# Optimization experiments

Hardware: AMD Instinct MI355X
Metric: run time of the kernel (lower is better)

## Reference

```python
import jax, jax.numpy as jnp
import numpy as np
from jax import lax

B, T, E, H, V = 1024, 128, 300, 100, 50000
K = 4  # topk in catch()
NEG_INF = -1e30


def setup_inputs() -> dict:
    key = jax.random.key(0)
    ks = jax.random.split(key, 12)
    word_id = jax.random.randint(ks[0], (B, T), 0, V, dtype=jnp.int32)
    sen_len = jax.random.randint(ks[1], (B,), K, T + 1, dtype=jnp.int32)  # >= K for topk
    label_word_id = jax.random.randint(ks[2], (B, 1), 0, V, dtype=jnp.int32)
    emb = jax.random.normal(ks[3], (V, E), jnp.float32) * 0.1
    W_ih = jax.random.normal(ks[4], (4 * H, E), jnp.float32) * 0.05
    W_hh = jax.random.normal(ks[5], (4 * H, H), jnp.float32) * 0.05
    b_ih = jax.random.normal(ks[6], (4 * H,), jnp.float32) * 0.05
    b_hh = jax.random.normal(ks[7], (4 * H,), jnp.float32) * 0.05
    lin_W = jax.random.normal(ks[8], (6, H), jnp.float32) * 0.1
    lin_b = jax.random.normal(ks[9], (6,), jnp.float32) * 0.1
    ll_W = jax.random.normal(ks[10], (H, E), jnp.float32) * 0.05
    ll_b = jax.random.normal(ks[11], (H,), jnp.float32) * 0.05
    return dict(word_id=word_id, sen_len=sen_len, label_word_id=label_word_id,
                emb=emb, W_ih=W_ih, W_hh=W_hh, b_ih=b_ih, b_hh=b_hh,
                lin_W=lin_W, lin_b=lin_b, ll_W=ll_W, ll_b=ll_b)


def _lstm(x, W_ih, W_hh, b_ih, b_hh):
    # x: (B, T, E) -> out: (B, T, H). Single layer, pytorch gate order i,f,g,o.
    b = b_ih + b_hh
    def step(carry, x_t):
        h, c = carry
        gates = x_t @ W_ih.T + h @ W_hh.T + b  # (B, 4H)
        i, f, g, o = jnp.split(gates, 4, axis=-1)
        c = jax.nn.sigmoid(f) * c + jax.nn.sigmoid(i) * jnp.tanh(g)
        h = jax.nn.sigmoid(o) * jnp.tanh(c)
        return (h, c), h
    h0 = jnp.zeros((x.shape[0], W_hh.shape[1]), x.dtype)
    (_, _), hs = lax.scan(step, (h0, h0), x.transpose(1, 0, 2))
    return hs.transpose(1, 0, 2)


def reference(word_id, sen_len, label_word_id, emb, W_ih, W_hh, b_ih, b_hh,
              lin_W, lin_b, ll_W, ll_b):
    word_vec = emb[word_id]                      # (B, T, E)
    out = _lstm(word_vec, W_ih, W_hh, b_ih, b_hh)  # (B, T, H)

    # last valid hidden state -> linear
    last = out[jnp.arange(out.shape[0]), sen_len - 1]  # (B, H)
    out_f = last @ lin_W.T + lin_b               # (B, 6)

    # label vector through llinear
    label_vec = emb[label_word_id[:, 0]] @ ll_W.T + ll_b  # (B, H)

    # --- catch(), vectorized ---
    scores = jnp.einsum('bth,bh->bt', out, label_vec)     # (B, T)
    valid = jnp.arange(out.shape[1])[None, :] < sen_len[:, None]  # (B, T)
    vals, idx = lax.top_k(jnp.where(valid, scores, NEG_INF), K)   # (B, K)
    s_value = jnp.take_along_axis(out, idx[:, :, None], axis=1)   # (B, K, H)
    pos = jnp.sum(s_value * vals[:, :, None], axis=1)             # (B, H)

    # neg: valid positions excluding topk; original bug: vector_list accumulates
    # across the batch loop -> cumulative sum over batch dimension.
    top_mask = jnp.zeros(valid.shape, bool).at[
        jnp.arange(valid.shape[0])[:, None], idx].set(True)
    neg_mask = valid & ~top_mask                                   # (B, T)
    per_neg = jnp.einsum('bth,bt->bh', out, neg_mask.astype(out.dtype))
    neg = jnp.cumsum(per_neg, axis=0)                              # (B, H)

    l_rep = pos @ lin_W.T + lin_b
    r_rep = neg @ lin_W.T + lin_b
    return (out_f, l_rep, r_rep)
```

## Files before the change

kernel.cpp:

```cpp
#include <hip/hip_runtime.h>
#include <hip/hip_bf16.h>
#include <cstdint>

#define Bn   1024
#define Tn   128
#define En   300
#define Hn   100
#define Vn   50000
#define G4n  400
#define MPn  50048
#define NPn  448

typedef __bf16 bf16x8 __attribute__((ext_vector_type(8)));
typedef _Float16 half8 __attribute__((ext_vector_type(8)));
typedef _Float16 half2v __attribute__((ext_vector_type(2)));
typedef float  f32x4  __attribute__((ext_vector_type(4)));

#define OFF_TABLE  0ull
#define OFF_OH16   44800000ull
#define OFF_WFRAG  71014400ull
#define OFF_WFRAGB 71129088ull
#define OFF_LLWT   71415808ull
#define OFF_LV     71535808ull
#define OFF_PN     71945408ull
#define OFF_NEG    72355008ull

__device__ __forceinline__ float sigf(float x) { return 1.0f / (1.0f + __expf(-x)); }
__device__ __forceinline__ float tanhfast(float x) { return 1.0f - 2.0f / (__expf(2.0f * x) + 1.0f); }

#define BAR_LDS() do {                                         \
    asm volatile("s_waitcnt lgkmcnt(0)" ::: "memory");          \
    __builtin_amdgcn_s_barrier();                               \
    asm volatile("" ::: "memory");                              \
} while (0)

#define DPP_ADD_SHL(v, N) do {                                                     \
    int _s = __builtin_amdgcn_update_dpp(0, __builtin_bit_cast(int, (v)),          \
                                         0x100 | (N), 0xF, 0xF, true);             \
    (v) += __builtin_bit_cast(float, _s);                                          \
} while (0)

__global__ void k_prep(const float* __restrict__ W_ih, const float* __restrict__ W_hh,
                       const float* __restrict__ llW,
                       uint4* __restrict__ wfrag, uint4* __restrict__ wfragB,
                       float* __restrict__ llwt) {
    int idx = blockIdx.x * 256 + threadIdx.x;
    if (idx < 28 * 4 * 64) {
        int lane = idx & 63, tk = idx >> 6;
        int nt = tk >> 2, kc = tk & 3;
        int n = nt * 16 + (lane & 15);
        int k0 = kc * 32 + (lane >> 4) * 8;
        int q = n & 3, u = n >> 2;
        union { _Float16 h[8]; uint4 v; } pk;
#pragma unroll
        for (int j = 0; j < 8; j++) {
            int k = k0 + j;
            pk.h[j] = (_Float16)((u < Hn && k < Hn) ? W_hh[(size_t)(q * Hn + u) * Hn + k] : 0.0f);
        }
        wfrag[idx] = pk.v;
    }
    if (idx < 10 * 28 * 64) {
        int lane = idx & 63, tk = idx >> 6;
        int kc = tk / 28, nsg = tk - kc * 28;
        int n = nsg * 16 + (lane & 15);
        int k0 = kc * 32 + (lane >> 4) * 8;
        int q = n & 3, u = n >> 2;
        union { __bf16 h[8]; uint4 v; } pk;
#pragma unroll
        for (int j = 0; j < 8; j++) {
            int k = k0 + j;
            pk.h[j] = (__bf16)((u < Hn && k < En) ? W_ih[(size_t)(q * Hn + u) * En + k] : 0.0f);
        }
        wfragB[idx] = pk.v;
    }
    if (idx < En * Hn) {
        int k = idx / Hn, h = idx - k * Hn;
        llwt[idx] = llW[(size_t)h * En + k];
    }
}

__global__ __launch_bounds__(256, 2) void k_table(
    const float* __restrict__ emb, const uint4* __restrict__ wfragB,
    const float* __restrict__ b_ih, const float* __restrict__ b_hh,
    _Float16* __restrict__ table) {
    __shared__ __bf16 a_sh[64][328];
    const int tid = threadIdx.x;
    const int mt = blockIdx.x >> 1, nh = blockIdx.x & 1;

#pragma unroll
    for (int it = 0; it < 5; it++) {
        int x = it * 256 + tid;
        int row = x / 20, seg = x - row * 20;
        int gr = mt * 64 + row;
        const float* ar = emb + (size_t)(gr < Vn ? gr : Vn - 1) * En;
        int c0 = seg * 16;
        union { __bf16 h[16]; bf16x8 v[2]; } pk;
#pragma unroll
        for (int g = 0; g < 4; g++) {
            int c = c0 + g * 4;
            if (c + 4 <= En) {
                float4 f = *(const float4*)(ar + c);
                pk.h[g * 4 + 0] = (__bf16)f.x; pk.h[g * 4 + 1] = (__bf16)f.y;
                pk.h[g * 4 + 2] = (__bf16)f.z; pk.h[g * 4 + 3] = (__bf16)f.w;
            } else {
                pk.h[g * 4 + 0] = (__bf16)0.f; pk.h[g * 4 + 1] = (__bf16)0.f;
                pk.h[g * 4 + 2] = (__bf16)0.f; pk.h[g * 4 + 3] = (__bf16)0.f;
            }
        }
        *(bf16x8*)&a_sh[row][c0] = pk.v[0];
        *(bf16x8*)&a_sh[row][c0 + 8] = pk.v[1];
    }
    __syncthreads();

    const int wv = tid >> 6, l = tid & 63;
    const int c16 = l & 15, quad = l >> 4;
    f32x4 acc[14];
#pragma unroll
    for (int i = 0; i < 14; i++) acc[i] = (f32x4){0.f, 0.f, 0.f, 0.f};

    uint4 bcur[14];
#pragma unroll
    for (int ns = 0; ns < 14; ns++) bcur[ns] = wfragB[((0 * 28 + nh * 14 + ns) << 6) + l];

    for (int kc = 0; kc < 10; kc++) {
        uint4 bnxt[14];
        if (kc < 9) {
#pragma unroll
            for (int ns = 0; ns < 14; ns++) bnxt[ns] = wfragB[(((kc + 1) * 28 + nh * 14 + ns) << 6) + l];
        }
        bf16x8 af = *(const bf16x8*)&a_sh[wv * 16 + c16][kc * 32 + quad * 8];
#pragma unroll
        for (int ns = 0; ns < 14; ns++)
            acc[ns] = __builtin_amdgcn_mfma_f32_16x16x32_bf16(af, __builtin_bit_cast(bf16x8, bcur[ns]), acc[ns], 0, 0, 0);
        if (kc < 9) {
#pragma unroll
            for (int ns = 0; ns < 14; ns++) bcur[ns] = bnxt[ns];
        }
    }
#pragma unroll
    for (int ns = 0; ns < 14; ns++) {
        int n = (nh * 14 + ns) * 16 + c16;
        int q = n & 3, u = n >> 2;
        if (u < Hn) {
            int j = q * Hn + u;
            float bias = b_ih[j] + b_hh[j];
#pragma unroll
            for (int r = 0; r < 4; r++) {
                int m = mt * 64 + wv * 16 + quad * 4 + r;
                if (m < Vn) table[(size_t)m * NPn + n] = (_Float16)(acc[ns][r] + bias);
            }
        }
    }
}

__global__ void k_label(const int* __restrict__ lwid, const float* __restrict__ emb,
                        const float* __restrict__ llwt, const float* __restrict__ llb,
                        float* __restrict__ lv) {
    __shared__ float er[En];
    __shared__ float part[Hn];
    int b = blockIdx.x;
    int lid = lwid[b];
    for (int k = threadIdx.x; k < En; k += 256) er[k] = emb[(size_t)lid * En + k];
    __syncthreads();
    int h = threadIdx.x & 127, half = threadIdx.x >> 7;
    float acc = 0.f;
    if (h < Hn) {
        int k0 = half * 150, k1 = k0 + 150;
        for (int k = k0; k < k1; k++) acc += er[k] * llwt[k * Hn + h];
        if (half == 1) part[h] = acc;
    }
    __syncthreads();
    if (h < Hn && half == 0) lv[(size_t)b * Hn + h] = acc + part[h] + llb[h];
}

__global__ __launch_bounds__(256, 2) void k_lstm(
    const int* __restrict__ word_id, const int* __restrict__ sen_len,
    const _Float16* __restrict__ table, const uint4* __restrict__ wfrag,
    const float* __restrict__ lv, const float* __restrict__ linW,
    const float* __restrict__ linb, _Float16* __restrict__ oh16,
    float* __restrict__ per_neg, float* __restrict__ d_out) {
    __shared__ float    gbufs[4][280];
    __shared__ _Float16 h_cur[2][2][136];
    __shared__ float    spw[2][Tn][16];
    __shared__ int      widc[2][Tn];
    __shared__ float    pos_sh[2][Hn];
    __shared__ float    lasth_sh[2][Hn];
    __shared__ float    tk_val[2][4];
    __shared__ int      tk_idx[2][4];

    const int tid = threadIdx.x;
    const int w = tid >> 6, l = tid & 63;
    const int c16 = l & 15, quad = l >> 4;
    const int b0 = blockIdx.x * 2;

    for (int i = tid; i < 272; i += 256) ((uint32_t*)h_cur)[i] = 0u;
    { int imb = tid >> 7, it = tid & 127; widc[imb][it] = word_id[(b0 + imb) * Tn + it]; }

    half8 bfr[7][4];
#pragma unroll
    for (int n7 = 0; n7 < 7; n7++)
#pragma unroll
        for (int kc = 0; kc < 4; kc++)
            bfr[n7][kc] = __builtin_bit_cast(half8, wfrag[((w * 7 + n7) * 4 + kc) * 64 + l]);

    const int u_loc = l >> 1, mb = l & 1;
    const int u = w * 28 + u_loc;
    const bool act = (l < 56) && (u < Hn);
    const int myslen = act ? sen_len[b0 + mb] : 0;
    const float lt_reg = act ? lv[(size_t)(b0 + mb) * Hn + u] : 0.f;
    float* gb = &gbufs[w][0];

    __syncthreads();

    uint2 xq = {0, 0}, xq1 = {0, 0};
    if (act) {
        xq  = *(const uint2*)(table + (size_t)widc[mb][0] * NPn + u * 4);
        xq1 = *(const uint2*)(table + (size_t)widc[mb][1] * NPn + u * 4);
    }

    float c_reg = 0.f, sumh = 0.f, lasth = 0.f;
    float p_carry = 0.f;
    _Float16* ohb_w = oh16 + (size_t)(b0 + mb) * Tn * Hn;

    for (int t = 0; t < Tn; t++) {
        const _Float16* hp = &h_cur[t & 1][0][0];
        f32x4 acc[7];
#pragma unroll
        for (int n7 = 0; n7 < 7; n7++) acc[n7] = (f32x4){0.f, 0.f, 0.f, 0.f};
#pragma unroll
        for (int kc = 0; kc < 4; kc++) {
            half8 af = *(const half8*)(hp + (c16 & 1) * 136 + kc * 32 + quad * 8);
#pragma unroll
            for (int n7 = 0; n7 < 7; n7++)
                acc[n7] = __builtin_amdgcn_mfma_f32_16x16x32_f16(af, bfr[n7][kc], acc[n7], 0, 0, 0);
        }
        {
            float pr = p_carry;
            DPP_ADD_SHL(pr, 2);
            DPP_ADD_SHL(pr, 4);
            DPP_ADD_SHL(pr, 8);
            if ((l & 15) < 2 && t > 0) spw[l & 1][t - 1][w * 4 + quad] = pr;
        }
        if (l < 16) {
#pragma unroll
            for (int n7 = 0; n7 < 7; n7++) {
                int nl = n7 * 16 + l;
                int adr = (nl >> 2) * 5 + (nl & 3);
                gb[adr] = acc[n7][0];
                gb[140 + adr] = acc[n7][1];
            }
        }
        float p = 0.f;
        if (act) {
            int base = mb * 140 + u_loc * 5;
            half2v x01 = __builtin_bit_cast(half2v, xq.x);
            half2v x23 = __builtin_bit_cast(half2v, xq.y);
            float gi = gb[base] + (float)x01.x;
            float gf = gb[base + 1] + (float)x01.y;
            float gg = gb[base + 2] + (float)x23.x;
            float go = gb[base + 3] + (float)x23.y;
            float c = sigf(gf) * c_reg + sigf(gi) * tanhfast(gg);
            c_reg = c;
            float hh = sigf(go) * tanhfast(c);
            h_cur[(t + 1) & 1][mb][u] = (_Float16)hh;
            ohb_w[t * Hn + u] = (_Float16)hh;
            if (t < myslen) sumh += hh;
            if (t == myslen - 1) lasth = hh;
            p = hh * lt_reg;
            int tn2 = (t + 2 < Tn) ? t + 2 : Tn - 1;
            xq = xq1;
            xq1 = *(const uint2*)(table + (size_t)widc[mb][tn2] * NPn + u * 4);
        }
        p_carry = p;
        BAR_LDS();
    }
    {
        float pr = p_carry;
        DPP_ADD_SHL(pr, 2);
        DPP_ADD_SHL(pr, 4);
        DPP_ADD_SHL(pr, 8);
        if ((l & 15) < 2) spw[l & 1][Tn - 1][w * 4 + quad] = pr;
    }
    __syncthreads();
    if (w < 2) {
        int kmb = w, lane = l;
        int sl = sen_len[b0 + kmb];
        const float* s16a = &spw[kmb][lane][0];
        const float* s16b = &spw[kmb][lane + 64][0];
        float4 a0 = *(const float4*)(s16a + 0), a1 = *(const float4*)(s16a + 4);
        float4 a2 = *(const float4*)(s16a + 8), a3 = *(const float4*)(s16a + 12);
        float4 b0v = *(const float4*)(s16b + 0), b1v = *(const float4*)(s16b + 4);
        float4 b2v = *(const float4*)(s16b + 8), b3v = *(const float4*)(s16b + 12);
        float sa = (a0.x + a0.y + a0.z + a0.w) + (a1.x + a1.y + a1.z + a1.w)
                 + (a2.x + a2.y + a2.z + a2.w) + (a3.x + a3.y + a3.z + a3.w);
        float sb = (b0v.x + b0v.y + b0v.z + b0v.w) + (b1v.x + b1v.y + b1v.z + b1v.w)
                 + (b2v.x + b2v.y + b2v.z + b2v.w) + (b3v.x + b3v.y + b3v.z + b3v.w);
        float s0 = (lane < sl) ? sa : -1e30f;
        float s1 = (lane + 64 < sl) ? sb : -1e30f;
        bool tk0 = false, tk1 = false;
#pragma unroll
        for (int p4 = 0; p4 < 4; p4++) {
            float v = tk0 ? -1e30f : s0;
            int ix = lane;
            float v1 = tk1 ? -1e30f : s1;
            if (v1 > v) { v = v1; ix = lane + 64; }
            for (int off = 32; off; off >>= 1) {
                float ov = __shfl_down(v, off, 64);
                int oi = __shfl_down(ix, off, 64);
                if (ov > v || (ov == v && oi < ix)) { v = ov; ix = oi; }
            }
            v = __shfl(v, 0, 64);
            ix = __shfl(ix, 0, 64);
            if (lane == 0) { tk_val[kmb][p4] = v; tk_idx[kmb][p4] = ix; }
            if (ix == lane) tk0 = true;
            if (ix == lane + 64) tk1 = true;
        }
    }
    __syncthreads();
    if (act) {
        float pos = 0.f, nsum = sumh;
#pragma unroll
        for (int p4 = 0; p4 < 4; p4++) {
            int ix = tk_idx[mb][p4];
            float r = (float)ohb_w[ix * Hn + u];
            pos += tk_val[mb][p4] * r;
            nsum -= r;
        }
        pos_sh[mb][u] = pos;
        lasth_sh[mb][u] = lasth;
        per_neg[(size_t)(b0 + mb) * Hn + u] = nsum;
    }
    __syncthreads();
    if (tid < 24) {
        int which = tid / 12, r = tid - which * 12;
        int pmb = r / 6, o = r - pmb * 6;
        const float* src = which ? &pos_sh[pmb][0] : &lasth_sh[pmb][0];
        float acc2 = linb[o];
        for (int uu = 0; uu < Hn; uu++) acc2 += src[uu] * linW[o * Hn + uu];
        d_out[(which ? (Bn * 6) : 0) + (b0 + pmb) * 6 + o] = acc2;
    }
}

__global__ __launch_bounds__(1024) void k_scan(const float* __restrict__ pn, float* __restrict__ neg) {
    __shared__ float wsum[16];
    __shared__ float wpre[16];
    int u = blockIdx.x, t = threadIdx.x;
    int lane = t & 63, wv = t >> 6;
    float v = pn[(size_t)t * Hn + u];
#pragma unroll
    for (int off = 1; off < 64; off <<= 1) {
        float o = __shfl_up(v, off, 64);
        if (lane >= off) v += o;
    }
    if (lane == 63) wsum[wv] = v;
    __syncthreads();
    if (t < 16) {
        float s = wsum[t];
#pragma unroll
        for (int off = 1; off < 16; off <<= 1) {
            float o = __shfl_up(s, off, 64);
            if (t >= off) s += o;
        }
        wpre[t] = s;
    }
    __syncthreads();
    float pre = wv ? wpre[wv - 1] : 0.f;
    neg[(size_t)t * Hn + u] = v + pre;
}

__global__ void k_rrep(const float* __restrict__ neg, const float* __restrict__ linW,
                       const float* __restrict__ linb, float* __restrict__ d_out) {
    int gid = blockIdx.x * 256 + threadIdx.x;
    if (gid < Bn * 6) {
        int b = gid / 6, o = gid - b * 6;
        float acc = linb[o];
        for (int u = 0; u < Hn; u++) acc += neg[(size_t)b * Hn + u] * linW[o * Hn + u];
        d_out[2 * Bn * 6 + gid] = acc;
    }
}

extern "C" void kernel_launch(void* const* d_in, const int* in_sizes, int n_in,
                              void* d_out, int out_size, void* d_ws, size_t ws_size,
                              hipStream_t stream) {
    const int*   word_id = (const int*)d_in[0];
    const int*   sen_len = (const int*)d_in[1];
    const int*   lwid    = (const int*)d_in[2];
    const float* emb     = (const float*)d_in[3];
    const float* W_ih    = (const float*)d_in[4];
    const float* W_hh    = (const float*)d_in[5];
    const float* b_ih    = (const float*)d_in[6];
    const float* b_hh    = (const float*)d_in[7];
    const float* linW    = (const float*)d_in[8];
    const float* linb    = (const float*)d_in[9];
    const float* llW     = (const float*)d_in[10];
    const float* llb     = (const float*)d_in[11];

    char* ws = (char*)d_ws;
    _Float16* table  = (_Float16*)(ws + OFF_TABLE);
    _Float16* oh16   = (_Float16*)(ws + OFF_OH16);
    uint4*    wfrag  = (uint4*)(ws + OFF_WFRAG);
    uint4*    wfragB = (uint4*)(ws + OFF_WFRAGB);
    float*    llwt   = (float*)(ws + OFF_LLWT);
    float*    lvp    = (float*)(ws + OFF_LV);
    float*    pn     = (float*)(ws + OFF_PN);
    float*    neg    = (float*)(ws + OFF_NEG);
    float*    outp   = (float*)d_out;

    k_prep<<<118, 256, 0, stream>>>(W_ih, W_hh, llW, wfrag, wfragB, llwt);
    k_table<<<(MPn / 64) * 2, 256, 0, stream>>>(emb, wfragB, b_ih, b_hh, table);
    k_label<<<Bn, 256, 0, stream>>>(lwid, emb, llwt, llb, lvp);
    k_lstm<<<Bn / 2, 256, 0, stream>>>(word_id, sen_len, table, wfrag, lvp, linW, linb, oh16, pn, outp);
    k_scan<<<Hn, 1024, 0, stream>>>(pn, neg);
    k_rrep<<<(Bn * 6 + 255) / 256, 256, 0, stream>>>(neg, linW, linb, outp);
}
```

Before: 309.1 us.

## Process four sequences per LSTM block to fill more MFMA rows

Each k_lstm block now handles four batch rows instead of two. It uses more rows of the 16-row MFMA A operand and halves the block count to 256, which fits one block per CU on a 256-CU part. Each active lane now runs the gate math for two sequences per timestep. The score buffer is transposed for the top-k reduction, and all four waves now do top-k. A large dummy shared array, written only under an impossible condition, forces LDS use up so blocks get one per CU. The cost is double the serial gate work per lane on the recurrent critical path.

```diff
diff --git a/kernel.cpp b/kernel.cpp
--- a/kernel.cpp
+++ b/kernel.cpp
@@ -173,28 +173,32 @@
     if (h < Hn && half == 0) lv[(size_t)b * Hn + h] = acc + part[h] + llb[h];
 }
 
-__global__ __launch_bounds__(256, 2) void k_lstm(
+__global__ __launch_bounds__(256, 1) void k_lstm(
     const int* __restrict__ word_id, const int* __restrict__ sen_len,
     const _Float16* __restrict__ table, const uint4* __restrict__ wfrag,
     const float* __restrict__ lv, const float* __restrict__ linW,
     const float* __restrict__ linb, _Float16* __restrict__ oh16,
     float* __restrict__ per_neg, float* __restrict__ d_out) {
-    __shared__ float    gbufs[4][280];
-    __shared__ _Float16 h_cur[2][2][136];
-    __shared__ float    spw[2][Tn][16];
-    __shared__ int      widc[2][Tn];
-    __shared__ float    pos_sh[2][Hn];
-    __shared__ float    lasth_sh[2][Hn];
-    __shared__ float    tk_val[2][4];
-    __shared__ int      tk_idx[2][4];
+    __shared__ float    gbufs[4][560];
+    __shared__ _Float16 h_cur[2][4][144];
+    __shared__ float    spw[4][16][132];
+    __shared__ int      widc[4][Tn];
+    __shared__ float    pos_sh[4][Hn];
+    __shared__ float    lasth_sh[4][Hn];
+    __shared__ float    tk_val[4][4];
+    __shared__ int      tk_idx[4][4];
+    __shared__ float    pad_force[9216];
 
     const int tid = threadIdx.x;
     const int w = tid >> 6, l = tid & 63;
     const int c16 = l & 15, quad = l >> 4;
-    const int b0 = blockIdx.x * 2;
-
-    for (int i = tid; i < 272; i += 256) ((uint32_t*)h_cur)[i] = 0u;
-    { int imb = tid >> 7, it = tid & 127; widc[imb][it] = word_id[(b0 + imb) * Tn + it]; }
+    const int b0 = blockIdx.x * 4;
+
+    if (__builtin_expect(sen_len[0] == -2147483647, 0)) pad_force[tid] = 1.f;
+
+    for (int i = tid; i < 576; i += 256) ((uint32_t*)h_cur)[i] = 0u;
+    for (int i = tid; i < 512; i += 256)
+        widc[i >> 7][i & 127] = word_id[(b0 + (i >> 7)) * Tn + (i & 127)];
 
     half8 bfr[7][4];
 #pragma unroll
@@ -203,24 +207,29 @@
         for (int kc = 0; kc < 4; kc++)
             bfr[n7][kc] = __builtin_bit_cast(half8, wfrag[((w * 7 + n7) * 4 + kc) * 64 + l]);
 
-    const int u_loc = l >> 1, mb = l & 1;
+    const int u_loc = l >> 1, sub = l & 1;
     const int u = w * 28 + u_loc;
     const bool act = (l < 56) && (u < Hn);
-    const int myslen = act ? sen_len[b0 + mb] : 0;
-    const float lt_reg = act ? lv[(size_t)(b0 + mb) * Hn + u] : 0.f;
+    const int slen_a = act ? sen_len[b0 + sub] : 0;
+    const int slen_b = act ? sen_len[b0 + sub + 2] : 0;
+    const float lt_a = act ? lv[(size_t)(b0 + sub) * Hn + u] : 0.f;
+    const float lt_b = act ? lv[(size_t)(b0 + sub + 2) * Hn + u] : 0.f;
     float* gb = &gbufs[w][0];
 
     __syncthreads();
 
-    uint2 xq = {0, 0}, xq1 = {0, 0};
+    uint2 xa0 = {0, 0}, xa1 = {0, 0}, xb0 = {0, 0}, xb1 = {0, 0};
     if (act) {
-        xq  = *(const uint2*)(table + (size_t)widc[mb][0] * NPn + u * 4);
-        xq1 = *(const uint2*)(table + (size_t)widc[mb][1] * NPn + u * 4);
-    }
-
-    float c_reg = 0.f, sumh = 0.f, lasth = 0.f;
-    float p_carry = 0.f;
-    _Float16* ohb_w = oh16 + (size_t)(b0 + mb) * Tn * Hn;
+        xa0 = *(const uint2*)(table + (size_t)widc[sub][0] * NPn + u * 4);
+        xa1 = *(const uint2*)(table + (size_t)widc[sub][1] * NPn + u * 4);
+        xb0 = *(const uint2*)(table + (size_t)widc[sub + 2][0] * NPn + u * 4);
+        xb1 = *(const uint2*)(table + (size_t)widc[sub + 2][1] * NPn + u * 4);
+    }
+
+    float ca = 0.f, cb = 0.f, sum_a = 0.f, sum_b = 0.f, last_a = 0.f, last_b = 0.f;
+    float pca = 0.f, pcb = 0.f;
+    _Float16* oha = oh16 + (size_t)(b0 + sub) * Tn * Hn;
+    _Float16* ohb = oh16 + (size_t)(b0 + sub + 2) * Tn * Hn;
 
     for (int t = 0; t < Tn; t++) {
         const _Float16* hp = &h_cur[t & 1][0][0];
@@ -229,81 +238,97 @@
         for (int n7 = 0; n7 < 7; n7++) acc[n7] = (f32x4){0.f, 0.f, 0.f, 0.f};
 #pragma unroll
         for (int kc = 0; kc < 4; kc++) {
-            half8 af = *(const half8*)(hp + (c16 & 1) * 136 + kc * 32 + quad * 8);
+            half8 af = *(const half8*)(hp + (c16 & 3) * 144 + kc * 32 + quad * 8);
 #pragma unroll
             for (int n7 = 0; n7 < 7; n7++)
                 acc[n7] = __builtin_amdgcn_mfma_f32_16x16x32_f16(af, bfr[n7][kc], acc[n7], 0, 0, 0);
         }
         {
-            float pr = p_carry;
-            DPP_ADD_SHL(pr, 2);
-            DPP_ADD_SHL(pr, 4);
-            DPP_ADD_SHL(pr, 8);
-            if ((l & 15) < 2 && t > 0) spw[l & 1][t - 1][w * 4 + quad] = pr;
+            float pra = pca, prb = pcb;
+            DPP_ADD_SHL(pra, 2); DPP_ADD_SHL(pra, 4); DPP_ADD_SHL(pra, 8);
+            DPP_ADD_SHL(prb, 2); DPP_ADD_SHL(prb, 4); DPP_ADD_SHL(prb, 8);
+            if ((l & 15) < 2 && t > 0) {
+                spw[l & 1][w * 4 + quad][t - 1] = pra;
+                spw[2 + (l & 1)][w * 4 + quad][t - 1] = prb;
+            }
         }
         if (l < 16) {
 #pragma unroll
             for (int n7 = 0; n7 < 7; n7++) {
                 int nl = n7 * 16 + l;
                 int adr = (nl >> 2) * 5 + (nl & 3);
-                gb[adr] = acc[n7][0];
+                gb[adr]       = acc[n7][0];
                 gb[140 + adr] = acc[n7][1];
+                gb[280 + adr] = acc[n7][2];
+                gb[420 + adr] = acc[n7][3];
             }
         }
-        float p = 0.f;
         if (act) {
-            int base = mb * 140 + u_loc * 5;
-            half2v x01 = __builtin_bit_cast(half2v, xq.x);
-            half2v x23 = __builtin_bit_cast(half2v, xq.y);
-            float gi = gb[base] + (float)x01.x;
-            float gf = gb[base + 1] + (float)x01.y;
-            float gg = gb[base + 2] + (float)x23.x;
-            float go = gb[base + 3] + (float)x23.y;
-            float c = sigf(gf) * c_reg + sigf(gi) * tanhfast(gg);
-            c_reg = c;
-            float hh = sigf(go) * tanhfast(c);
-            h_cur[(t + 1) & 1][mb][u] = (_Float16)hh;
-            ohb_w[t * Hn + u] = (_Float16)hh;
-            if (t < myslen) sumh += hh;
-            if (t == myslen - 1) lasth = hh;
-            p = hh * lt_reg;
+            int base = sub * 140 + u_loc * 5;
+            half2v a01 = __builtin_bit_cast(half2v, xa0.x);
+            half2v a23 = __builtin_bit_cast(half2v, xa0.y);
+            float gia = gb[base] + (float)a01.x;
+            float gfa = gb[base + 1] + (float)a01.y;
+            float gga = gb[base + 2] + (float)a23.x;
+            float goa = gb[base + 3] + (float)a23.y;
+            ca = sigf(gfa) * ca + sigf(gia) * tanhfast(gga);
+            float ha = sigf(goa) * tanhfast(ca);
+            h_cur[(t + 1) & 1][sub][u] = (_Float16)ha;
+            oha[t * Hn + u] = (_Float16)ha;
+            if (t < slen_a) sum_a += ha;
+            if (t == slen_a - 1) last_a = ha;
+            int baseb = base + 280;
+            half2v b01 = __builtin_bit_cast(half2v, xb0.x);
+            half2v b23 = __builtin_bit_cast(half2v, xb0.y);
+            float gib = gb[baseb] + (float)b01.x;
+            float gfb = gb[baseb + 1] + (float)b01.y;
+            float ggb = gb[baseb + 2] + (float)b23.x;
+            float gob = gb[baseb + 3] + (float)b23.y;
+            cb = sigf(gfb) * cb + sigf(gib) * tanhfast(ggb);
+            float hb = sigf(gob) * tanhfast(cb);
+            h_cur[(t + 1) & 1][sub + 2][u] = (_Float16)hb;
+            ohb[t * Hn + u] = (_Float16)hb;
+            if (t < slen_b) sum_b += hb;
+            if (t == slen_b - 1) last_b = hb;
+            pca = ha * lt_a;
+            pcb = hb * lt_b;
             int tn2 = (t + 2 < Tn) ? t + 2 : Tn - 1;
-            xq = xq1;
-            xq1 = *(const uint2*)(table + (size_t)widc[mb][tn2] * NPn + u * 4);
-        }
-        p_carry = p;
+            xa0 = xa1;
+            xa1 = *(const uint2*)(table + (size_t)widc[sub][tn2] * NPn + u * 4);
+            xb0 = xb1;
+            xb1 = *(const uint2*)(table + (size_t)widc[sub + 2][tn2] * NPn + u * 4);
+        } else {
+            pca = 0.f; pcb = 0.f;
+        }
         BAR_LDS();
     }
     {
-        float pr = p_carry;
-        DPP_ADD_SHL(pr, 2);
-        DPP_ADD_SHL(pr, 4);
-        DPP_ADD_SHL(pr, 8);
-        if ((l & 15) < 2) spw[l & 1][Tn - 1][w * 4 + quad] = pr;
-    }
-    __syncthreads();
-    if (w < 2) {
-        int kmb = w, lane = l;
-        int sl = sen_len[b0 + kmb];
-        const float* s16a = &spw[kmb][lane][0];
-        const float* s16b = &spw[kmb][lane + 64][0];
-        float4 a0 = *(const float4*)(s16a + 0), a1 = *(const float4*)(s16a + 4);
-        float4 a2 = *(const float4*)(s16a + 8), a3 = *(const float4*)(s16a + 12);
-        float4 b0v = *(const float4*)(s16b + 0), b1v = *(const float4*)(s16b + 4);
-        float4 b2v = *(const float4*)(s16b + 8), b3v = *(const float4*)(s16b + 12);
-        float sa = (a0.x + a0.y + a0.z + a0.w) + (a1.x + a1.y + a1.z + a1.w)
-                 + (a2.x + a2.y + a2.z + a2.w) + (a3.x + a3.y + a3.z + a3.w);
-        float sb = (b0v.x + b0v.y + b0v.z + b0v.w) + (b1v.x + b1v.y + b1v.z + b1v.w)
-                 + (b2v.x + b2v.y + b2v.z + b2v.w) + (b3v.x + b3v.y + b3v.z + b3v.w);
-        float s0 = (lane < sl) ? sa : -1e30f;
-        float s1 = (lane + 64 < sl) ? sb : -1e30f;
+        float pra = pca, prb = pcb;
+        DPP_ADD_SHL(pra, 2); DPP_ADD_SHL(pra, 4); DPP_ADD_SHL(pra, 8);
+        DPP_ADD_SHL(prb, 2); DPP_ADD_SHL(prb, 4); DPP_ADD_SHL(prb, 8);
+        if ((l & 15) < 2) {
+            spw[l & 1][w * 4 + quad][Tn - 1] = pra;
+            spw[2 + (l & 1)][w * 4 + quad][Tn - 1] = prb;
+        }
+    }
+    __syncthreads();
+    {
+        int sl = sen_len[b0 + w];
+        float s0 = 0.f, s1 = 0.f;
+#pragma unroll
+        for (int j = 0; j < 16; j++) {
+            s0 += spw[w][j][l];
+            s1 += spw[w][j][l + 64];
+        }
+        if (l >= sl) s0 = -1e30f;
+        if (l + 64 >= sl) s1 = -1e30f;
         bool tk0 = false, tk1 = false;
 #pragma unroll
         for (int p4 = 0; p4 < 4; p4++) {
             float v = tk0 ? -1e30f : s0;
-            int ix = lane;
+            int ix = l;
             float v1 = tk1 ? -1e30f : s1;
-            if (v1 > v) { v = v1; ix = lane + 64; }
+            if (v1 > v) { v = v1; ix = l + 64; }
             for (int off = 32; off; off >>= 1) {
                 float ov = __shfl_down(v, off, 64);
                 int oi = __shfl_down(ix, off, 64);
@@ -311,28 +336,36 @@
             }
             v = __shfl(v, 0, 64);
             ix = __shfl(ix, 0, 64);
-            if (lane == 0) { tk_val[kmb][p4] = v; tk_idx[kmb][p4] = ix; }
-            if (ix == lane) tk0 = true;
-            if (ix == lane + 64) tk1 = true;
+            if (l == 0) { tk_val[w][p4] = v; tk_idx[w][p4] = ix; }
+            if (ix == l) tk0 = true;
+            if (ix == l + 64) tk1 = true;
         }
     }
     __syncthreads();
     if (act) {
-        float pos = 0.f, nsum = sumh;
+        float pos_a = 0.f, ns_a = sum_a;
+        float pos_b = 0.f, ns_b = sum_b;
 #pragma unroll
         for (int p4 = 0; p4 < 4; p4++) {
-            int ix = tk_idx[mb][p4];
-            float r = (float)ohb_w[ix * Hn + u];
-            pos += tk_val[mb][p4] * r;
-            nsum -= r;
-        }
-        pos_sh[mb][u] = pos;
-        lasth_sh[mb][u] = lasth;
-        per_neg[(size_t)(b0 + mb) * Hn + u] = nsum;
-    }
-    __syncthreads();
-    if (tid < 24) {
-        int which = tid / 12, r = tid - which * 12;
+            int ixa = tk_idx[sub][p4];
+            float ra = (float)oha[ixa * Hn + u];
+            pos_a += tk_val[sub][p4] * ra;
+            ns_a -= ra;
+            int ixb = tk_idx[sub + 2][p4];
+            float rb = (float)ohb[ixb * Hn + u];
+            pos_b += tk_val[sub + 2][p4] * rb;
+            ns_b -= rb;
+        }
+        pos_sh[sub][u] = pos_a;
+        lasth_sh[sub][u] = last_a;
+        per_neg[(size_t)(b0 + sub) * Hn + u] = ns_a;
+        pos_sh[sub + 2][u] = pos_b;
+        lasth_sh[sub + 2][u] = last_b;
+        per_neg[(size_t)(b0 + sub + 2) * Hn + u] = ns_b;
+    }
+    __syncthreads();
+    if (tid < 48) {
+        int which = tid / 24, r = tid - which * 24;
         int pmb = r / 6, o = r - pmb * 6;
         const float* src = which ? &pos_sh[pmb][0] : &lasth_sh[pmb][0];
         float acc2 = linb[o];
@@ -409,7 +442,7 @@
     k_prep<<<118, 256, 0, stream>>>(W_ih, W_hh, llW, wfrag, wfragB, llwt);
     k_table<<<(MPn / 64) * 2, 256, 0, stream>>>(emb, wfragB, b_ih, b_hh, table);
     k_label<<<Bn, 256, 0, stream>>>(lwid, emb, llwt, llb, lvp);
-    k_lstm<<<Bn / 2, 256, 0, stream>>>(word_id, sen_len, table, wfrag, lvp, linW, linb, oh16, pn, outp);
+    k_lstm<<<Bn / 4, 256, 0, stream>>>(word_id, sen_len, table, wfrag, lvp, linW, linb, oh16, pn, outp);
     k_scan<<<Hn, 1024, 0, stream>>>(pn, neg);
     k_rrep<<<(Bn * 6 + 255) / 256, 256, 0, stream>>>(neg, linW, linb, outp);
 }
```

Measured after the change: 326.3 us. 5.6% more time.

## Keep LSTM outputs in LDS and scan projected negatives instead of hidden sums

Applied to the files above, without the earlier changes.

The per-step hidden outputs now go to a shared-memory buffer instead of a global fp16 scratch array, which removes global writes and re-reads for the top-k gather. The neg cumulative sum is reordered by linearity: each block projects its per-batch negative sum through lin_W first, so the scan works on 6 columns instead of 100, and the separate r_rep kernel is dropped. The sigmoid and tanh helpers use hardware reciprocal, and the gate-buffer stores are moved ahead of the DPP reduction. Shared memory per block grows by about 51KB, which may limit occupancy under the two-blocks-per-CU launch bound. Reordering the projection and the cumsum also changes floating-point summation order slightly.

```diff
diff --git a/kernel.cpp b/kernel.cpp
--- a/kernel.cpp
+++ b/kernel.cpp
@@ -17,16 +17,18 @@
 typedef float  f32x4  __attribute__((ext_vector_type(4)));
 
 #define OFF_TABLE  0ull
-#define OFF_OH16   44800000ull
-#define OFF_WFRAG  71014400ull
-#define OFF_WFRAGB 71129088ull
-#define OFF_LLWT   71415808ull
-#define OFF_LV     71535808ull
-#define OFF_PN     71945408ull
-#define OFF_NEG    72355008ull
-
-__device__ __forceinline__ float sigf(float x) { return 1.0f / (1.0f + __expf(-x)); }
-__device__ __forceinline__ float tanhfast(float x) { return 1.0f - 2.0f / (__expf(2.0f * x) + 1.0f); }
+#define OFF_WFRAG  44800000ull
+#define OFF_WFRAGB 44914688ull
+#define OFF_LLWT   45201408ull
+#define OFF_LV     45321408ull
+#define OFF_PN6    45731008ull
+
+__device__ __forceinline__ float sigf(float x) {
+    return __builtin_amdgcn_rcpf(1.0f + __expf(-x));
+}
+__device__ __forceinline__ float tanhfast(float x) {
+    return 1.0f - 2.0f * __builtin_amdgcn_rcpf(__expf(2.0f * x) + 1.0f);
+}
 
 #define BAR_LDS() do {                                         \
     asm volatile("s_waitcnt lgkmcnt(0)" ::: "memory");          \
@@ -177,14 +179,16 @@
     const int* __restrict__ word_id, const int* __restrict__ sen_len,
     const _Float16* __restrict__ table, const uint4* __restrict__ wfrag,
     const float* __restrict__ lv, const float* __restrict__ linW,
-    const float* __restrict__ linb, _Float16* __restrict__ oh16,
-    float* __restrict__ per_neg, float* __restrict__ d_out) {
+    const float* __restrict__ linb, float* __restrict__ pn6,
+    float* __restrict__ d_out) {
     __shared__ float    gbufs[4][280];
     __shared__ _Float16 h_cur[2][2][136];
+    __shared__ _Float16 oh_lds[2][12832];
     __shared__ float    spw[2][Tn][16];
     __shared__ int      widc[2][Tn];
     __shared__ float    pos_sh[2][Hn];
     __shared__ float    lasth_sh[2][Hn];
+    __shared__ float    neg_sh[2][Hn];
     __shared__ float    tk_val[2][4];
     __shared__ int      tk_idx[2][4];
 
@@ -194,7 +198,7 @@
     const int b0 = blockIdx.x * 2;
 
     for (int i = tid; i < 272; i += 256) ((uint32_t*)h_cur)[i] = 0u;
-    { int imb = tid >> 7, it = tid & 127; widc[imb][it] = word_id[(b0 + imb) * Tn + it]; }
+    { int imb = tid >> 7, it = tid & 127; widc[imb][it] = word_id[(b0 + imb) * Tn + it] * NPn; }
 
     half8 bfr[7][4];
 #pragma unroll
@@ -209,30 +213,44 @@
     const int myslen = act ? sen_len[b0 + mb] : 0;
     const float lt_reg = act ? lv[(size_t)(b0 + mb) * Hn + u] : 0.f;
     float* gb = &gbufs[w][0];
+    const _Float16* tb_u = table + u * 4;
 
     __syncthreads();
 
     uint2 xq = {0, 0}, xq1 = {0, 0};
     if (act) {
-        xq  = *(const uint2*)(table + (size_t)widc[mb][0] * NPn + u * 4);
-        xq1 = *(const uint2*)(table + (size_t)widc[mb][1] * NPn + u * 4);
+        xq  = *(const uint2*)(tb_u + (size_t)widc[mb][0]);
+        xq1 = *(const uint2*)(tb_u + (size_t)widc[mb][1]);
     }
 
     float c_reg = 0.f, sumh = 0.f, lasth = 0.f;
     float p_carry = 0.f;
-    _Float16* ohb_w = oh16 + (size_t)(b0 + mb) * Tn * Hn;
 
     for (int t = 0; t < Tn; t++) {
         const _Float16* hp = &h_cur[t & 1][0][0];
         f32x4 acc[7];
-#pragma unroll
-        for (int n7 = 0; n7 < 7; n7++) acc[n7] = (f32x4){0.f, 0.f, 0.f, 0.f};
-#pragma unroll
-        for (int kc = 0; kc < 4; kc++) {
+        {
+            half8 af0 = *(const half8*)(hp + (c16 & 1) * 136 + quad * 8);
+#pragma unroll
+            for (int n7 = 0; n7 < 7; n7++)
+                acc[n7] = __builtin_amdgcn_mfma_f32_16x16x32_f16(
+                    af0, bfr[n7][0], (f32x4){0.f, 0.f, 0.f, 0.f}, 0, 0, 0);
+        }
+#pragma unroll
+        for (int kc = 1; kc < 4; kc++) {
             half8 af = *(const half8*)(hp + (c16 & 1) * 136 + kc * 32 + quad * 8);
 #pragma unroll
             for (int n7 = 0; n7 < 7; n7++)
                 acc[n7] = __builtin_amdgcn_mfma_f32_16x16x32_f16(af, bfr[n7][kc], acc[n7], 0, 0, 0);
+        }
+        if (l < 16) {
+#pragma unroll
+            for (int n7 = 0; n7 < 7; n7++) {
+                int nl = n7 * 16 + l;
+                int adr = (nl >> 2) * 5 + (nl & 3);
+                gb[adr] = acc[n7][0];
+                gb[140 + adr] = acc[n7][1];
+            }
         }
         {
             float pr = p_carry;
@@ -240,15 +258,6 @@
             DPP_ADD_SHL(pr, 4);
             DPP_ADD_SHL(pr, 8);
             if ((l & 15) < 2 && t > 0) spw[l & 1][t - 1][w * 4 + quad] = pr;
-        }
-        if (l < 16) {
-#pragma unroll
-            for (int n7 = 0; n7 < 7; n7++) {
-                int nl = n7 * 16 + l;
-                int adr = (nl >> 2) * 5 + (nl & 3);
-                gb[adr] = acc[n7][0];
-                gb[140 + adr] = acc[n7][1];
-            }
         }
         float p = 0.f;
         if (act) {
@@ -262,14 +271,15 @@
             float c = sigf(gf) * c_reg + sigf(gi) * tanhfast(gg);
             c_reg = c;
             float hh = sigf(go) * tanhfast(c);
-            h_cur[(t + 1) & 1][mb][u] = (_Float16)hh;
-            ohb_w[t * Hn + u] = (_Float16)hh;
+            _Float16 h16 = (_Float16)hh;
+            h_cur[(t + 1) & 1][mb][u] = h16;
+            oh_lds[mb][t * Hn + u] = h16;
             if (t < myslen) sumh += hh;
             if (t == myslen - 1) lasth = hh;
             p = hh * lt_reg;
             int tn2 = (t + 2 < Tn) ? t + 2 : Tn - 1;
             xq = xq1;
-            xq1 = *(const uint2*)(table + (size_t)widc[mb][tn2] * NPn + u * 4);
+            xq1 = *(const uint2*)(tb_u + (size_t)widc[mb][tn2]);
         }
         p_carry = p;
         BAR_LDS();
@@ -322,35 +332,40 @@
 #pragma unroll
         for (int p4 = 0; p4 < 4; p4++) {
             int ix = tk_idx[mb][p4];
-            float r = (float)ohb_w[ix * Hn + u];
+            float r = (float)oh_lds[mb][ix * Hn + u];
             pos += tk_val[mb][p4] * r;
             nsum -= r;
         }
         pos_sh[mb][u] = pos;
         lasth_sh[mb][u] = lasth;
-        per_neg[(size_t)(b0 + mb) * Hn + u] = nsum;
-    }
-    __syncthreads();
-    if (tid < 24) {
+        neg_sh[mb][u] = nsum;
+    }
+    __syncthreads();
+    if (tid < 36) {
         int which = tid / 12, r = tid - which * 12;
         int pmb = r / 6, o = r - pmb * 6;
-        const float* src = which ? &pos_sh[pmb][0] : &lasth_sh[pmb][0];
-        float acc2 = linb[o];
+        const float* src = (which == 0) ? &lasth_sh[pmb][0]
+                         : (which == 1) ? &pos_sh[pmb][0] : &neg_sh[pmb][0];
+        float acc2 = (which == 2) ? 0.f : linb[o];
         for (int uu = 0; uu < Hn; uu++) acc2 += src[uu] * linW[o * Hn + uu];
-        d_out[(which ? (Bn * 6) : 0) + (b0 + pmb) * 6 + o] = acc2;
-    }
-}
-
-__global__ __launch_bounds__(1024) void k_scan(const float* __restrict__ pn, float* __restrict__ neg) {
+        if (which == 0)      d_out[(b0 + pmb) * 6 + o] = acc2;
+        else if (which == 1) d_out[Bn * 6 + (b0 + pmb) * 6 + o] = acc2;
+        else                 pn6[(b0 + pmb) * 6 + o] = acc2;
+    }
+}
+
+__global__ __launch_bounds__(1024) void k_scan6(const float* __restrict__ pn6,
+                                                const float* __restrict__ linb,
+                                                float* __restrict__ d_out) {
     __shared__ float wsum[16];
     __shared__ float wpre[16];
-    int u = blockIdx.x, t = threadIdx.x;
+    int o = blockIdx.x, t = threadIdx.x;
     int lane = t & 63, wv = t >> 6;
-    float v = pn[(size_t)t * Hn + u];
+    float v = pn6[t * 6 + o];
 #pragma unroll
     for (int off = 1; off < 64; off <<= 1) {
-        float o = __shfl_up(v, off, 64);
-        if (lane >= off) v += o;
+        float x = __shfl_up(v, off, 64);
+        if (lane >= off) v += x;
     }
     if (lane == 63) wsum[wv] = v;
     __syncthreads();
@@ -358,25 +373,14 @@
         float s = wsum[t];
 #pragma unroll
         for (int off = 1; off < 16; off <<= 1) {
-            float o = __shfl_up(s, off, 64);
-            if (t >= off) s += o;
+            float x = __shfl_up(s, off, 64);
+            if (t >= off) s += x;
         }
         wpre[t] = s;
     }
     __syncthreads();
     float pre = wv ? wpre[wv - 1] : 0.f;
-    neg[(size_t)t * Hn + u] = v + pre;
-}
-
-__global__ void k_rrep(const float* __restrict__ neg, const float* __restrict__ linW,
-                       const float* __restrict__ linb, float* __restrict__ d_out) {
-    int gid = blockIdx.x * 256 + threadIdx.x;
-    if (gid < Bn * 6) {
-        int b = gid / 6, o = gid - b * 6;
-        float acc = linb[o];
-        for (int u = 0; u < Hn; u++) acc += neg[(size_t)b * Hn + u] * linW[o * Hn + u];
-        d_out[2 * Bn * 6 + gid] = acc;
-    }
+    d_out[2 * Bn * 6 + t * 6 + o] = v + pre + linb[o];
 }
 
 extern "C" void kernel_launch(void* const* d_in, const int* in_sizes, int n_in,
@@ -397,19 +401,16 @@
 
     char* ws = (char*)d_ws;
     _Float16* table  = (_Float16*)(ws + OFF_TABLE);
-    _Float16* oh16   = (_Float16*)(ws + OFF_OH16);
     uint4*    wfrag  = (uint4*)(ws + OFF_WFRAG);
     uint4*    wfragB = (uint4*)(ws + OFF_WFRAGB);
     float*    llwt   = (float*)(ws + OFF_LLWT);
     float*    lvp    = (float*)(ws + OFF_LV);
-    float*    pn     = (float*)(ws + OFF_PN);
-    float*    neg    = (float*)(ws + OFF_NEG);
+    float*    pn6    = (float*)(ws + OFF_PN6);
     float*    outp   = (float*)d_out;
 
     k_prep<<<118, 256, 0, stream>>>(W_ih, W_hh, llW, wfrag, wfragB, llwt);
     k_table<<<(MPn / 64) * 2, 256, 0, stream>>>(emb, wfragB, b_ih, b_hh, table);
     k_label<<<Bn, 256, 0, stream>>>(lwid, emb, llwt, llb, lvp);
-    k_lstm<<<Bn / 2, 256, 0, stream>>>(word_id, sen_len, table, wfrag, lvp, linW, linb, oh16, pn, outp);
-    k_scan<<<Hn, 1024, 0, stream>>>(pn, neg);
-    k_rrep<<<(Bn * 6 + 255) / 256, 256, 0, stream>>>(neg, linW, linb, outp);
-}
+    k_lstm<<<Bn / 2, 256, 0, stream>>>(word_id, sen_len, table, wfrag, lvp, linW, linb, pn6, outp);
+    k_scan6<<<6, 1024, 0, stream>>>(pn6, linb, outp);
+}
```

Measured after the change: 278.8 us. 9.8% less time.
